# Kernel tuning notes

Hardware: AMD Instinct MI355X
Metric: run time of the kernel (lower is better)

Reference implementation:

```python
import jax, jax.numpy as jnp
import numpy as np

N_HEAD = 8
LN_EPS = 1e-6


def setup_inputs() -> dict:
    key = jax.random.key(0)
    ks = jax.random.split(key, 6)
    B, S, D = 4, 2048, 256  # D = hidden_size*2 = input_dim
    sc = 1.0 / np.sqrt(D)
    return {
        "inputs": jax.random.normal(ks[0], (B, S, D), jnp.float32),
        "Wq": jax.random.normal(ks[1], (D, D), jnp.float32) * sc,
        "Wk": jax.random.normal(ks[2], (D, D), jnp.float32) * sc,
        "Wv": jax.random.normal(ks[3], (D, D), jnp.float32) * sc,
        "Wf": jax.random.normal(ks[4], (D, D), jnp.float32) * sc,
        "bf": jnp.zeros((D,), jnp.float32),
        "gamma": jnp.ones((D,), jnp.float32),
        "beta": jnp.zeros((D,), jnp.float32),
    }


def reference(inputs, Wq, Wk, Wv, Wf, bf, gamma, beta):
    B, S, D = inputs.shape
    H = N_HEAD
    dh = D // H
    # Projections (torch Linear: x @ W.T), no bias for Q/K/V
    Q = (inputs @ Wq.T).reshape(B, S, H, dh)
    K = (inputs @ Wk.T).reshape(B, S, H, dh)
    V = (inputs @ Wv.T).reshape(B, S, H, dh)
    # NOTE: original scales by sqrt(K.shape[1]) == sqrt(seq_len), not sqrt(dh)
    scale = 1.0 / jnp.sqrt(jnp.float32(S)).astype(inputs.dtype)
    scores = jnp.einsum("bqhd,bkhd->bhqk", Q, K) * scale  # [B,H,S,S]
    attn = jax.nn.softmax(scores, axis=-1)
    out = jnp.einsum("bhqk,bkhd->bqhd", attn, V).reshape(B, S, D)
    out = out @ Wf.T + bf
    # residual + LayerNorm(eps=1e-6)
    x = inputs + out
    mu = jnp.mean(x, axis=-1, keepdims=True)
    var = jnp.mean(jnp.square(x - mu), axis=-1, keepdims=True)
    return (x - mu) * jax.lax.rsqrt(var + LN_EPS) * gamma + beta
```

## Files before the change

kernel.cpp:

```cpp
#include <hip/hip_runtime.h>
#include <hip/hip_bf16.h>

typedef __attribute__((ext_vector_type(8))) short short8;
typedef __attribute__((ext_vector_type(4))) float f32x4;
typedef __attribute__((ext_vector_type(16))) float f32x16;

#define DEVI __device__ __forceinline__

DEVI unsigned short f2bf(float f) {
  union { float f; unsigned int u; } v; v.f = f;
  unsigned int r = v.u + 0x7fffu + ((v.u >> 16) & 1u);
  return (unsigned short)(r >> 16);
}

DEVI unsigned int cvt2(float lo, float hi) {
  unsigned int r;
  asm("v_cvt_pk_bf16_f32 %0, %1, %2" : "=v"(r) : "v"(lo), "v"(hi));
  return r;
}

#define GLDS16(gp, lp)                                                         \
  __builtin_amdgcn_global_load_lds(                                            \
      (const __attribute__((address_space(1))) unsigned int*)(uintptr_t)(gp),  \
      (__attribute__((address_space(3))) unsigned int*)(uintptr_t)(lp), 16, 0, 0)

#define SB 4
#define SS 2048
#define SD 256
#define SH 8
#define SDH 32
#define SM 8192

#define QSCALE 0.0318793654f

#define Q_OFF   0
#define K_OFF   (SM * SD)
#define VT_OFF  (2 * SM * SD)
#define AO_OFF  (3 * SM * SD)
#define WF_OFF  (4 * SM * SD)

__global__ __launch_bounds__(256) void qkv_k(
    const float* __restrict__ X, const float* __restrict__ Wq,
    const float* __restrict__ Wk, const float* __restrict__ Wv,
    const float* __restrict__ Wf, unsigned short* __restrict__ ws) {
  __shared__ __align__(16) unsigned short Atile[64][72];
  __shared__ __align__(16) unsigned short Btile[128][72];
  int tid = threadIdx.x, w = tid >> 6, lane = tid & 63, g = lane >> 4, r = lane & 15;
  int m0 = blockIdx.x * 64;
  int z = blockIdx.y >> 1, nbase = (blockIdx.y & 1) * 128;
  const float* Wz = (z == 0) ? Wq : (z == 1) ? Wk : Wv;
  if (z == 2) {
    int slice = blockIdx.x + (nbase ? 128 : 0);
    ws[WF_OFF + slice * 256 + tid] = f2bf(Wf[slice * 256 + tid]);
  }
  int wr = (w >> 1) * 32, wc = (w & 1) * 64;
  f32x4 acc[2][4] = {};
  int srow = tid >> 3, scol = (tid & 7) * 8;
  float4 a0[2], a1[2], b0[4], b1[4];
#pragma unroll
  for (int p = 0; p < 2; ++p) {
    const float* xa = X + (m0 + srow + p * 32) * SD + scol;
    a0[p] = *reinterpret_cast<const float4*>(xa);
    a1[p] = *reinterpret_cast<const float4*>(xa + 4);
  }
#pragma unroll
  for (int p = 0; p < 4; ++p) {
    const float* xb = Wz + (nbase + srow + p * 32) * SD + scol;
    b0[p] = *reinterpret_cast<const float4*>(xb);
    b1[p] = *reinterpret_cast<const float4*>(xb + 4);
  }
  for (int k0 = 0; k0 < SD; k0 += 64) {
    __syncthreads();
#pragma unroll
    for (int p = 0; p < 2; ++p) {
      uint4 ua = { cvt2(a0[p].x, a0[p].y), cvt2(a0[p].z, a0[p].w),
                   cvt2(a1[p].x, a1[p].y), cvt2(a1[p].z, a1[p].w) };
      *reinterpret_cast<uint4*>(&Atile[srow + p * 32][scol]) = ua;
    }
#pragma unroll
    for (int p = 0; p < 4; ++p) {
      uint4 ub = { cvt2(b0[p].x, b0[p].y), cvt2(b0[p].z, b0[p].w),
                   cvt2(b1[p].x, b1[p].y), cvt2(b1[p].z, b1[p].w) };
      *reinterpret_cast<uint4*>(&Btile[srow + p * 32][scol]) = ub;
    }
    __syncthreads();
    if (k0 + 64 < SD) {
#pragma unroll
      for (int p = 0; p < 2; ++p) {
        const float* xa = X + (m0 + srow + p * 32) * SD + k0 + 64 + scol;
        a0[p] = *reinterpret_cast<const float4*>(xa);
        a1[p] = *reinterpret_cast<const float4*>(xa + 4);
      }
#pragma unroll
      for (int p = 0; p < 4; ++p) {
        const float* xb = Wz + (nbase + srow + p * 32) * SD + k0 + 64 + scol;
        b0[p] = *reinterpret_cast<const float4*>(xb);
        b1[p] = *reinterpret_cast<const float4*>(xb + 4);
      }
    }
#pragma unroll
    for (int ks = 0; ks < 2; ++ks) {
      short8 af[2], bf[4];
#pragma unroll
      for (int i = 0; i < 2; ++i)
        af[i] = *reinterpret_cast<const short8*>(&Atile[wr + i * 16 + r][ks * 32 + g * 8]);
#pragma unroll
      for (int j = 0; j < 4; ++j)
        bf[j] = *reinterpret_cast<const short8*>(&Btile[wc + j * 16 + r][ks * 32 + g * 8]);
#pragma unroll
      for (int i = 0; i < 2; ++i)
#pragma unroll
        for (int j = 0; j < 4; ++j)
          acc[i][j] = __builtin_amdgcn_mfma_f32_16x16x32_bf16(af[i], bf[j], acc[i][j], 0, 0, 0);
    }
  }
  int b_ = m0 >> 11, sbase = m0 & 2047;
  float qs = (z == 0) ? QSCALE : 1.0f;
  unsigned short* Vt = &Btile[0][0];
#pragma unroll
  for (int p = 0; p < 2; ++p) {
    __syncthreads();
    if ((w & 1) == p) {
      if (z < 2) {
#pragma unroll
        for (int i = 0; i < 2; ++i)
#pragma unroll
          for (int j = 0; j < 4; ++j)
#pragma unroll
            for (int jj = 0; jj < 4; ++jj)
              Atile[wr + i * 16 + g * 4 + jj][j * 16 + r] = f2bf(acc[i][j][jj] * qs);
      } else {
#pragma unroll
        for (int i = 0; i < 2; ++i)
#pragma unroll
          for (int j = 0; j < 4; ++j) {
            unsigned short o4[4];
#pragma unroll
            for (int jj = 0; jj < 4; ++jj) o4[jj] = f2bf(acc[i][j][jj]);
            *reinterpret_cast<uint2*>(&Vt[(j * 16 + r) * 80 + wr + i * 16 + g * 4]) =
                *reinterpret_cast<const uint2*>(o4);
          }
      }
    }
    __syncthreads();
    if (z < 2) {
      unsigned short* out = ws + (z == 0 ? Q_OFF : K_OFF);
      int h0 = (nbase + p * 64) >> 5;
#pragma unroll
      for (int it = 0; it < 2; ++it) {
        int c = it * 256 + tid;
        int m = c >> 3, cr = c & 7, hl = cr >> 2, ch = cr & 3;
        short8 val = *reinterpret_cast<const short8*>(&Atile[m][hl * 32 + ch * 8]);
        int h = h0 + hl;
        *reinterpret_cast<short8*>(
            out + (((b_ << 3) + h) * SS + sbase + m) * SDH + ch * 8) = val;
      }
    } else {
      unsigned short* out = ws + VT_OFF;
      int nb = nbase + p * 64;
#pragma unroll
      for (int it = 0; it < 2; ++it) {
        int c = it * 256 + tid;
        int nl = c >> 3, ch = c & 7;
        short8 val = *reinterpret_cast<const short8*>(&Vt[nl * 80 + ch * 8]);
        int col = nb + nl, h = col >> 5, d = col & 31;
        *reinterpret_cast<short8*>(
            out + ((((b_ << 3) + h) << 5) + d) * SS + sbase + ch * 8) = val;
      }
    }
  }
}

__global__ __launch_bounds__(512, 4) void attn_k(const unsigned short* __restrict__ ws_c,
                                                 unsigned short* __restrict__ ws) {
  __shared__ __align__(16) unsigned char smem[65536];
  int tid = threadIdx.x, w = tid >> 6, lane = tid & 63;
  int wg = w >> 2, wl = w & 3, gtid = tid & 255;
  int n32 = lane & 31, hi = lane >> 5;
  int wgid = ((blockIdx.x & 7) << 6) + (blockIdx.x >> 3);
  int bh = wgid >> 4, qb = wgid & 15;
  int q0 = qb * 128 + wl * 32;
  const unsigned short* Qh = ws_c + Q_OFF + bh * (SS * SDH);
  const unsigned short* Kg = ws_c + K_OFF + (bh * SS + wg * 1024) * SDH;
  const unsigned short* Vg = ws_c + VT_OFF + bh * (SDH * SS) + wg * 1024;
  short8 qB0 = *reinterpret_cast<const short8*>(Qh + (q0 + n32) * SDH + 8 * hi);
  short8 qB1 = *reinterpret_cast<const short8*>(Qh + (q0 + n32) * SDH + 16 + 8 * hi);
  unsigned short* Kbuf0 = (unsigned short*)(smem + wg * 16384);
  unsigned short* Kbuf1 = (unsigned short*)(smem + wg * 16384 + 8192);
  unsigned short* Vbuf0 = (unsigned short*)(smem + 32768 + wg * 16384);
  unsigned short* Vbuf1 = (unsigned short*)(smem + 32768 + wg * 16384 + 8192);
  int wv = gtid >> 6;
  int kr = gtid >> 2;
  int kcg = (gtid & 3) ^ ((kr >> 1) & 3);
  const unsigned short* gK0 = Kg + kr * SDH + kcg * 8;
  const unsigned short* gK1 = gK0 + 64 * SDH;
  int vr = gtid >> 4;
  int vcg = (gtid & 15) ^ (vr & 7);
  const unsigned short* gV0 = Vg + vr * SS + vcg * 8;
  const unsigned short* gV1 = gV0 + 16 * SS;
  auto issue = [&](int buf, int tt) {
    char* kd = (char*)(buf ? Kbuf1 : Kbuf0) + wv * 1024;
    char* vd = (char*)(buf ? Vbuf1 : Vbuf0) + wv * 1024;
    GLDS16(gK0 + tt * 4096, kd);
    GLDS16(gK1 + tt * 4096, kd + 4096);
    GLDS16(gV0 + tt * 128, vd);
    GLDS16(gV1 + tt * 128, vd + 4096);
  };
  issue(0, 0);
  f32x16 O = {}, Lf = {};
  union { unsigned int u[4]; short8 sv; } ONES;
  ONES.u[0] = 0x3F803F80u; ONES.u[1] = 0x3F803F80u;
  ONES.u[2] = 0x3F803F80u; ONES.u[3] = 0x3F803F80u;
  int rb = (n32 >> 1) & 3;
  int koff0 = (hi ^ rb) * 8;
  int koff1 = ((2 + hi) ^ rb) * 8;
  int vb7 = n32 & 7;
  for (int t = 0; t < 8; ++t) {
    const unsigned short* Kt = (t & 1) ? Kbuf1 : Kbuf0;
    const unsigned short* Vt = (t & 1) ? Vbuf1 : Vbuf0;
    if (t < 7) {
      issue((t + 1) & 1, t + 1);
      asm volatile("s_waitcnt vmcnt(4)" ::: "memory");
    } else {
      asm volatile("s_waitcnt vmcnt(0)" ::: "memory");
    }
    __builtin_amdgcn_s_barrier();
#pragma unroll
    for (int si = 0; si < 4; ++si) {
      int s = (si + wl) & 3;
      const unsigned short* krow = Kt + (s * 32 + n32) * 32;
      short8 ka = *reinterpret_cast<const short8*>(krow + koff0);
      short8 kb = *reinterpret_cast<const short8*>(krow + koff1);
      f32x16 aC = {};
      __builtin_amdgcn_s_setprio(1);
      aC = __builtin_amdgcn_mfma_f32_32x32x16_bf16(ka, qB0, aC, 0, 0, 0);
      aC = __builtin_amdgcn_mfma_f32_32x32x16_bf16(kb, qB1, aC, 0, 0, 0);
      __builtin_amdgcn_s_setprio(0);
#pragma unroll
      for (int i = 0; i < 16; ++i) aC[i] = __builtin_amdgcn_exp2f(aC[i]);
      unsigned int pk[8];
#pragma unroll
      for (int i = 0; i < 8; ++i) pk[i] = cvt2(aC[2 * i], aC[2 * i + 1]);
      asm("v_permlane32_swap_b32 %0, %1" : "+v"(pk[0]), "+v"(pk[2]));
      asm("v_permlane32_swap_b32 %0, %1" : "+v"(pk[1]), "+v"(pk[3]));
      asm("v_permlane32_swap_b32 %0, %1" : "+v"(pk[4]), "+v"(pk[6]));
      asm("v_permlane32_swap_b32 %0, %1" : "+v"(pk[5]), "+v"(pk[7]));
      union { unsigned int u[4]; short8 sv; } A1, A2;
      A1.u[0] = pk[0]; A1.u[1] = pk[1]; A1.u[2] = pk[2]; A1.u[3] = pk[3];
      A2.u[0] = pk[4]; A2.u[1] = pk[5]; A2.u[2] = pk[6]; A2.u[3] = pk[7];
      const unsigned short* vrow = Vt + n32 * 128;
      short8 vB0 = *reinterpret_cast<const short8*>(vrow + ((s * 4 + hi) ^ vb7) * 8);
      short8 vB1 = *reinterpret_cast<const short8*>(vrow + ((s * 4 + 2 + hi) ^ vb7) * 8);
      __builtin_amdgcn_s_setprio(1);
      O  = __builtin_amdgcn_mfma_f32_32x32x16_bf16(A1.sv, vB0, O, 0, 0, 0);
      O  = __builtin_amdgcn_mfma_f32_32x32x16_bf16(A2.sv, vB1, O, 0, 0, 0);
      Lf = __builtin_amdgcn_mfma_f32_32x32x16_bf16(A1.sv, ONES.sv, Lf, 0, 0, 0);
      Lf = __builtin_amdgcn_mfma_f32_32x32x16_bf16(A2.sv, ONES.sv, Lf, 0, 0, 0);
      __builtin_amdgcn_s_setprio(0);
    }
    __builtin_amdgcn_s_barrier();
  }
  __syncthreads();
  float* OCf = reinterpret_cast<float*>(smem);
  float* LCf = OCf + 16 * 257;
  int p = wl * 64 + lane;
  if (wg == 1) {
#pragma unroll
    for (int i = 0; i < 16; ++i) { OCf[i * 257 + p] = O[i]; LCf[i * 257 + p] = Lf[i]; }
  }
  __syncthreads();
  if (wg == 0) {
    int b = bh >> 3, h = bh & 7;
    unsigned short* AO = ws + AO_OFF;
#pragma unroll
    for (int rr = 0; rr < 16; ++rr) {
      float Ot = O[rr] + OCf[rr * 257 + p];
      float Lt = Lf[rr] + LCf[rr * 257 + p];
      int q = (rr & 3) + 8 * (rr >> 2) + 4 * hi;
      AO[(b * SS + q0 + q) * SD + h * SDH + n32] = f2bf(Ot / Lt);
    }
  }
}

__global__ __launch_bounds__(256) void final_k(
    const unsigned short* __restrict__ ws_c, const float* __restrict__ X,
    const float* __restrict__ bfv, const float* __restrict__ gamma,
    const float* __restrict__ beta, float* __restrict__ out) {
  __shared__ __align__(16) unsigned short Al[16][72];
  __shared__ __align__(16) unsigned short Bl[256][72];
  __shared__ float Cl[16][257];
  const unsigned short* AO = ws_c + AO_OFF;
  const unsigned short* Wfb = ws_c + WF_OFF;
  int tid = threadIdx.x, w = tid >> 6, lane = tid & 63, g = lane >> 4, r = lane & 15;
  int m0 = blockIdx.x * 16;
  f32x4 acc[4] = {};
  int arow = tid >> 4, acol = (tid & 15) * 4;
  int brow = tid >> 3, bcol = (tid & 7) * 8;
  for (int k0 = 0; k0 < SD; k0 += 64) {
    uint2 av = *reinterpret_cast<const uint2*>(AO + (m0 + arow) * SD + k0 + acol);
    short8 bv[8];
#pragma unroll
    for (int i = 0; i < 8; i++)
      bv[i] = *reinterpret_cast<const short8*>(Wfb + (i * 32 + brow) * SD + k0 + bcol);
    __syncthreads();
    *reinterpret_cast<uint2*>(&Al[arow][acol]) = av;
#pragma unroll
    for (int i = 0; i < 8; i++)
      *reinterpret_cast<short8*>(&Bl[i * 32 + brow][bcol]) = bv[i];
    __syncthreads();
#pragma unroll
    for (int ks = 0; ks < 2; ks++) {
      short8 af = *reinterpret_cast<const short8*>(&Al[r][ks * 32 + g * 8]);
#pragma unroll
      for (int nt = 0; nt < 4; nt++) {
        short8 bb = *reinterpret_cast<const short8*>(&Bl[w * 64 + nt * 16 + r][ks * 32 + g * 8]);
        acc[nt] = __builtin_amdgcn_mfma_f32_16x16x32_bf16(af, bb, acc[nt], 0, 0, 0);
      }
    }
  }
#pragma unroll
  for (int nt = 0; nt < 4; nt++)
#pragma unroll
    for (int j = 0; j < 4; j++)
      Cl[g * 4 + j][w * 64 + nt * 16 + r] = acc[nt][j];
  __syncthreads();
  int row = tid >> 4, sub = tid & 15;
  int m = m0 + row;
  float x[16];
  float sum = 0.f, sumsq = 0.f;
#pragma unroll
  for (int i = 0; i < 4; i++) {
    int col = sub * 16 + i * 4;
    float4 xv = *reinterpret_cast<const float4*>(X + m * SD + col);
    float4 bb = *reinterpret_cast<const float4*>(bfv + col);
    x[i * 4 + 0] = Cl[row][col + 0] + xv.x + bb.x;
    x[i * 4 + 1] = Cl[row][col + 1] + xv.y + bb.y;
    x[i * 4 + 2] = Cl[row][col + 2] + xv.z + bb.z;
    x[i * 4 + 3] = Cl[row][col + 3] + xv.w + bb.w;
  }
#pragma unroll
  for (int c = 0; c < 16; c++) { sum += x[c]; sumsq += x[c] * x[c]; }
  sum += __shfl_xor(sum, 1);  sumsq += __shfl_xor(sumsq, 1);
  sum += __shfl_xor(sum, 2);  sumsq += __shfl_xor(sumsq, 2);
  sum += __shfl_xor(sum, 4);  sumsq += __shfl_xor(sumsq, 4);
  sum += __shfl_xor(sum, 8);  sumsq += __shfl_xor(sumsq, 8);
  float mean = sum * (1.0f / 256.0f);
  float var = sumsq * (1.0f / 256.0f) - mean * mean;
  float rstd = rsqrtf(var + 1e-6f);
#pragma unroll
  for (int i = 0; i < 4; i++) {
    int col = sub * 16 + i * 4;
    float4 gv = *reinterpret_cast<const float4*>(gamma + col);
    float4 bv2 = *reinterpret_cast<const float4*>(beta + col);
    float4 ov;
    ov.x = (x[i * 4 + 0] - mean) * rstd * gv.x + bv2.x;
    ov.y = (x[i * 4 + 1] - mean) * rstd * gv.y + bv2.y;
    ov.z = (x[i * 4 + 2] - mean) * rstd * gv.z + bv2.z;
    ov.w = (x[i * 4 + 3] - mean) * rstd * gv.w + bv2.w;
    *reinterpret_cast<float4*>(out + m * SD + col) = ov;
  }
}

extern "C" void kernel_launch(void* const* d_in, const int* in_sizes, int n_in,
                              void* d_out, int out_size, void* d_ws, size_t ws_size,
                              hipStream_t stream) {
  const float* X  = (const float*)d_in[0];
  const float* Wq = (const float*)d_in[1];
  const float* Wk = (const float*)d_in[2];
  const float* Wv = (const float*)d_in[3];
  const float* Wf = (const float*)d_in[4];
  const float* bf = (const float*)d_in[5];
  const float* gm = (const float*)d_in[6];
  const float* bt = (const float*)d_in[7];
  float* out = (float*)d_out;
  unsigned short* ws = (unsigned short*)d_ws;

  qkv_k<<<dim3(128, 6), 256, 0, stream>>>(X, Wq, Wk, Wv, Wf, ws);
  attn_k<<<dim3(512), 512, 0, stream>>>(ws, ws);
  final_k<<<512, 256, 0, stream>>>(ws, X, bf, gm, bt, out);
}
```

Baseline: 54.77 us.

## Pre-convert inputs to bf16 and double-buffer QKV GEMM with async LDS loads

Adds a separate conversion kernel that writes X and all four weight matrices to bf16 in the workspace. The QKV projection kernel then streams bf16 tiles straight into LDS through global_load_lds into XOR-swizzled double buffers, overlapping the next tile's load with the current MFMA work. This removes the in-register fp32-to-bf16 conversion and the register staging from the GEMM loop. The cost is an extra kernel launch and an extra full pass over X (fp32 read plus bf16 write and re-read).

```diff
diff --git a/kernel.cpp b/kernel.cpp
--- a/kernel.cpp
+++ b/kernel.cpp
@@ -30,6 +30,7 @@
 #define SH 8
 #define SDH 32
 #define SM 8192
+#define WN (SD * SD)
 
 #define QSCALE 0.0318793654f
 
@@ -37,86 +38,84 @@
 #define K_OFF   (SM * SD)
 #define VT_OFF  (2 * SM * SD)
 #define AO_OFF  (3 * SM * SD)
-#define WF_OFF  (4 * SM * SD)
-
-__global__ __launch_bounds__(256) void qkv_k(
+#define XB_OFF  (4 * SM * SD)
+#define W_OFF   (5 * SM * SD)
+
+__global__ __launch_bounds__(256) void convert_k(
     const float* __restrict__ X, const float* __restrict__ Wq,
     const float* __restrict__ Wk, const float* __restrict__ Wv,
     const float* __restrict__ Wf, unsigned short* __restrict__ ws) {
-  __shared__ __align__(16) unsigned short Atile[64][72];
-  __shared__ __align__(16) unsigned short Btile[128][72];
+  const int XN = SM * SD;
+  int i4 = (blockIdx.x * 256 + threadIdx.x) * 4;
+  const float* src; unsigned short* dst; int idx;
+  if (i4 < XN)             { src = X;  dst = ws + XB_OFF;       idx = i4; }
+  else if (i4 < XN + WN)   { src = Wq; dst = ws + W_OFF;        idx = i4 - XN; }
+  else if (i4 < XN + 2*WN) { src = Wk; dst = ws + W_OFF + WN;   idx = i4 - XN - WN; }
+  else if (i4 < XN + 3*WN) { src = Wv; dst = ws + W_OFF + 2*WN; idx = i4 - XN - 2*WN; }
+  else if (i4 < XN + 4*WN) { src = Wf; dst = ws + W_OFF + 3*WN; idx = i4 - XN - 3*WN; }
+  else return;
+  float4 v = *reinterpret_cast<const float4*>(src + idx);
+  unsigned short o[4] = { f2bf(v.x), f2bf(v.y), f2bf(v.z), f2bf(v.w) };
+  *reinterpret_cast<uint2*>(dst + idx) = *reinterpret_cast<const uint2*>(o);
+}
+
+__global__ __launch_bounds__(256) void qkv_k(const unsigned short* __restrict__ ws_c,
+                                             unsigned short* __restrict__ ws) {
+  __shared__ __align__(16) unsigned short Ab[2][64 * 64];
+  __shared__ __align__(16) unsigned short Bb[2][128 * 64];
   int tid = threadIdx.x, w = tid >> 6, lane = tid & 63, g = lane >> 4, r = lane & 15;
   int m0 = blockIdx.x * 64;
   int z = blockIdx.y >> 1, nbase = (blockIdx.y & 1) * 128;
-  const float* Wz = (z == 0) ? Wq : (z == 1) ? Wk : Wv;
-  if (z == 2) {
-    int slice = blockIdx.x + (nbase ? 128 : 0);
-    ws[WF_OFF + slice * 256 + tid] = f2bf(Wf[slice * 256 + tid]);
-  }
+  const unsigned short* Xb = ws_c + XB_OFF;
+  const unsigned short* Wall = ws_c + W_OFF + (z * 256 + nbase) * SD;
+  int lr = lane >> 3, lc = lane & 7;
+  int cg = lc ^ lr;
+  const unsigned short* srcA = Xb + (m0 + w * 16 + lr) * SD + cg * 8;
+  const unsigned short* srcB = Wall + (w * 32 + lr) * SD + cg * 8;
+  auto stage = [&](int buf, int k0) {
+    unsigned short* da = &Ab[buf][w * 1024];
+    unsigned short* db = &Bb[buf][w * 2048];
+#pragma unroll
+    for (int j = 0; j < 2; ++j) GLDS16(srcA + j * 8 * SD + k0, da + j * 512);
+#pragma unroll
+    for (int j = 0; j < 4; ++j) GLDS16(srcB + j * 8 * SD + k0, db + j * 512);
+  };
+  stage(0, 0);
   int wr = (w >> 1) * 32, wc = (w & 1) * 64;
   f32x4 acc[2][4] = {};
-  int srow = tid >> 3, scol = (tid & 7) * 8;
-  float4 a0[2], a1[2], b0[4], b1[4];
-#pragma unroll
-  for (int p = 0; p < 2; ++p) {
-    const float* xa = X + (m0 + srow + p * 32) * SD + scol;
-    a0[p] = *reinterpret_cast<const float4*>(xa);
-    a1[p] = *reinterpret_cast<const float4*>(xa + 4);
-  }
-#pragma unroll
-  for (int p = 0; p < 4; ++p) {
-    const float* xb = Wz + (nbase + srow + p * 32) * SD + scol;
-    b0[p] = *reinterpret_cast<const float4*>(xb);
-    b1[p] = *reinterpret_cast<const float4*>(xb + 4);
-  }
-  for (int k0 = 0; k0 < SD; k0 += 64) {
-    __syncthreads();
-#pragma unroll
-    for (int p = 0; p < 2; ++p) {
-      uint4 ua = { cvt2(a0[p].x, a0[p].y), cvt2(a0[p].z, a0[p].w),
-                   cvt2(a1[p].x, a1[p].y), cvt2(a1[p].z, a1[p].w) };
-      *reinterpret_cast<uint4*>(&Atile[srow + p * 32][scol]) = ua;
-    }
-#pragma unroll
-    for (int p = 0; p < 4; ++p) {
-      uint4 ub = { cvt2(b0[p].x, b0[p].y), cvt2(b0[p].z, b0[p].w),
-                   cvt2(b1[p].x, b1[p].y), cvt2(b1[p].z, b1[p].w) };
-      *reinterpret_cast<uint4*>(&Btile[srow + p * 32][scol]) = ub;
-    }
-    __syncthreads();
-    if (k0 + 64 < SD) {
-#pragma unroll
-      for (int p = 0; p < 2; ++p) {
-        const float* xa = X + (m0 + srow + p * 32) * SD + k0 + 64 + scol;
-        a0[p] = *reinterpret_cast<const float4*>(xa);
-        a1[p] = *reinterpret_cast<const float4*>(xa + 4);
-      }
-#pragma unroll
-      for (int p = 0; p < 4; ++p) {
-        const float* xb = Wz + (nbase + srow + p * 32) * SD + k0 + 64 + scol;
-        b0[p] = *reinterpret_cast<const float4*>(xb);
-        b1[p] = *reinterpret_cast<const float4*>(xb + 4);
-      }
-    }
+  int ks0 = (g ^ (r & 7)) * 8;
+  int ks1 = ((4 + g) ^ (r & 7)) * 8;
+  for (int step = 0; step < 4; ++step) {
+    if (step < 3) {
+      stage((step + 1) & 1, (step + 1) * 64);
+      asm volatile("s_waitcnt vmcnt(6)" ::: "memory");
+    } else {
+      asm volatile("s_waitcnt vmcnt(0)" ::: "memory");
+    }
+    __builtin_amdgcn_s_barrier();
+    const unsigned short* At = &Ab[step & 1][0];
+    const unsigned short* Bt = &Bb[step & 1][0];
 #pragma unroll
     for (int ks = 0; ks < 2; ++ks) {
+      int co = ks ? ks1 : ks0;
       short8 af[2], bf[4];
 #pragma unroll
       for (int i = 0; i < 2; ++i)
-        af[i] = *reinterpret_cast<const short8*>(&Atile[wr + i * 16 + r][ks * 32 + g * 8]);
+        af[i] = *reinterpret_cast<const short8*>(At + (wr + i * 16 + r) * 64 + co);
 #pragma unroll
       for (int j = 0; j < 4; ++j)
-        bf[j] = *reinterpret_cast<const short8*>(&Btile[wc + j * 16 + r][ks * 32 + g * 8]);
+        bf[j] = *reinterpret_cast<const short8*>(Bt + (wc + j * 16 + r) * 64 + co);
 #pragma unroll
       for (int i = 0; i < 2; ++i)
 #pragma unroll
         for (int j = 0; j < 4; ++j)
           acc[i][j] = __builtin_amdgcn_mfma_f32_16x16x32_bf16(af[i], bf[j], acc[i][j], 0, 0, 0);
     }
+    __builtin_amdgcn_s_barrier();
   }
   int b_ = m0 >> 11, sbase = m0 & 2047;
   float qs = (z == 0) ? QSCALE : 1.0f;
-  unsigned short* Vt = &Btile[0][0];
+  unsigned short* Ct = &Ab[0][0];
 #pragma unroll
   for (int p = 0; p < 2; ++p) {
     __syncthreads();
@@ -128,7 +127,7 @@
           for (int j = 0; j < 4; ++j)
 #pragma unroll
             for (int jj = 0; jj < 4; ++jj)
-              Atile[wr + i * 16 + g * 4 + jj][j * 16 + r] = f2bf(acc[i][j][jj] * qs);
+              Ct[(wr + i * 16 + g * 4 + jj) * 72 + j * 16 + r] = f2bf(acc[i][j][jj] * qs);
       } else {
 #pragma unroll
         for (int i = 0; i < 2; ++i)
@@ -137,7 +136,7 @@
             unsigned short o4[4];
 #pragma unroll
             for (int jj = 0; jj < 4; ++jj) o4[jj] = f2bf(acc[i][j][jj]);
-            *reinterpret_cast<uint2*>(&Vt[(j * 16 + r) * 80 + wr + i * 16 + g * 4]) =
+            *reinterpret_cast<uint2*>(&Ct[(j * 16 + r) * 80 + wr + i * 16 + g * 4]) =
                 *reinterpret_cast<const uint2*>(o4);
           }
       }
@@ -150,7 +149,7 @@
       for (int it = 0; it < 2; ++it) {
         int c = it * 256 + tid;
         int m = c >> 3, cr = c & 7, hl = cr >> 2, ch = cr & 3;
-        short8 val = *reinterpret_cast<const short8*>(&Atile[m][hl * 32 + ch * 8]);
+        short8 val = *reinterpret_cast<const short8*>(&Ct[m * 72 + hl * 32 + ch * 8]);
         int h = h0 + hl;
         *reinterpret_cast<short8*>(
             out + (((b_ << 3) + h) * SS + sbase + m) * SDH + ch * 8) = val;
@@ -162,7 +161,7 @@
       for (int it = 0; it < 2; ++it) {
         int c = it * 256 + tid;
         int nl = c >> 3, ch = c & 7;
-        short8 val = *reinterpret_cast<const short8*>(&Vt[nl * 80 + ch * 8]);
+        short8 val = *reinterpret_cast<const short8*>(&Ct[nl * 80 + ch * 8]);
         int col = nb + nl, h = col >> 5, d = col & 31;
         *reinterpret_cast<short8*>(
             out + ((((b_ << 3) + h) << 5) + d) * SS + sbase + ch * 8) = val;
@@ -290,7 +289,7 @@
   __shared__ __align__(16) unsigned short Bl[256][72];
   __shared__ float Cl[16][257];
   const unsigned short* AO = ws_c + AO_OFF;
-  const unsigned short* Wfb = ws_c + WF_OFF;
+  const unsigned short* Wfb = ws_c + W_OFF + 3 * WN;
   int tid = threadIdx.x, w = tid >> 6, lane = tid & 63, g = lane >> 4, r = lane & 15;
   int m0 = blockIdx.x * 16;
   f32x4 acc[4] = {};
@@ -375,7 +374,8 @@
   float* out = (float*)d_out;
   unsigned short* ws = (unsigned short*)d_ws;
 
-  qkv_k<<<dim3(128, 6), 256, 0, stream>>>(X, Wq, Wk, Wv, Wf, ws);
+  convert_k<<<2304, 256, 0, stream>>>(X, Wq, Wk, Wv, Wf, ws);
+  qkv_k<<<dim3(128, 6), 256, 0, stream>>>(ws, ws);
   attn_k<<<dim3(512), 512, 0, stream>>>(ws, ws);
   final_k<<<512, 256, 0, stream>>>(ws, X, bf, gm, bt, out);
 }
```

After: 56.40 us. 3.0% more time.
